# Performance work log

Measured on AMD Instinct MI355X. Metric: run time of the kernel, lower is better.

The kernel has to match this reference:

```python
import jax, jax.numpy as jnp
import numpy as np

# dims
T, B = 1024, 64
IN, EMB, HID, K, OUT = 32, 64, 128, 16, 32


def setup_inputs() -> dict:
    key = jax.random.key(0)
    ks = jax.random.split(key, 16)
    s = 0.05
    f32 = jnp.float32
    return {
        "inputs": jax.random.normal(ks[0], (T, B, IN), f32),
        "W_emb": jax.random.normal(ks[1], (IN, EMB), f32) * s,
        "b_emb": jnp.zeros((EMB,), f32),
        # layer 0: gates packed as [i, o, c, d]
        "Wx0": jax.random.normal(ks[2], (EMB, 4 * HID), f32) * s,
        "Wh0": jax.random.normal(ks[3], (HID, 4 * HID), f32) * s,
        "b0": jnp.zeros((4 * HID,), f32),
        "Wo0": jax.random.normal(ks[4], (HID, HID), f32) * s,
        "bo0": jnp.zeros((HID,), f32),
        # layer 1 (last layer projects to output_size)
        "Wx1": jax.random.normal(ks[5], (HID, 4 * HID), f32) * s,
        "Wh1": jax.random.normal(ks[6], (HID, 4 * HID), f32) * s,
        "b1": jnp.zeros((4 * HID,), f32),
        "Wo1": jax.random.normal(ks[7], (HID, OUT), f32) * s,
        "bo1": jnp.zeros((OUT,), f32),
    }


def mlstm_layer(x_seq, Wx, Wh, b, Wo, bo):
    """One mLSTM layer scanned over time.

    x_seq: [T, B, Din]. Cell state is a k-truncated fractional filter:
      c_t = sum_{j=0}^{K-1} w_j(d_t) * hc_{t-j},  hc = i ⊙ tanh(c_gate)
      w_0 = 1, w_j = w_{j-1} * (j-1+d_t)/j   (coeffs of (1-B)^{-d})
      d_t = 0.5 * sigmoid(d_gate)  in (0, 0.5)
    """
    H = Wh.shape[0]
    Bsz = x_seq.shape[1]
    xg = x_seq @ Wx + b  # [T, B, 4H] input contribution, precomputed once
    j = jnp.arange(1, K, dtype=x_seq.dtype).reshape(K - 1, 1, 1)

    h0 = jnp.zeros((Bsz, H), x_seq.dtype)
    buf0 = jnp.zeros((K, Bsz, H), x_seq.dtype)  # newest candidate first

    def step(carry, xg_t):
        h, buf = carry
        g = xg_t + h @ Wh
        i_g, o_g, c_g, d_g = jnp.split(g, 4, axis=-1)
        i_g = jax.nn.sigmoid(i_g)
        o_g = jax.nn.sigmoid(o_g)
        d = 0.5 * jax.nn.sigmoid(d_g)            # [B, H] dynamic memory param
        hc = i_g * jnp.tanh(c_g)                 # gated candidate
        buf = jnp.concatenate([hc[None], buf[:-1]], axis=0)  # [K, B, H]
        # fractional-integration weights w_j(d), recursive product, vectorized
        w = jnp.concatenate(
            [jnp.ones((1, Bsz, H), buf.dtype),
             jnp.cumprod((j - 1.0 + d) / j, axis=0)], axis=0)  # [K, B, H]
        c = jnp.sum(w * buf, axis=0)
        h_new = o_g * jnp.tanh(c)
        out = h_new @ Wo + bo
        return (h_new, buf), out

    _, outs = jax.lax.scan(step, (h0, buf0), xg)
    return outs  # [T, B, Dout]


def reference(inputs, W_emb, b_emb, Wx0, Wh0, b0, Wo0, bo0, Wx1, Wh1, b1, Wo1, bo1):
    x = inputs @ W_emb + b_emb                    # input embedding
    x = mlstm_layer(x, Wx0, Wh0, b0, Wo0, bo0)    # layer 0 -> hidden_size
    return mlstm_layer(x, Wx1, Wh1, b1, Wo1, bo1) # layer 1 -> output_size
```

## Files before the change

### kernel.cpp

```cpp
#include <hip/hip_runtime.h>
#include <hip/hip_bf16.h>
#include <cstdint>
#include <type_traits>

#define T_DIM 1024
#define B_DIM 64
#define IN_DIM 32
#define EMB_DIM 64
#define HID_DIM 128
#define K_TAPS 16
#define OUT_DIM 32
#define G4 (4*HID_DIM)
#define MROWS (T_DIM*B_DIM)

typedef _Float16 half8 __attribute__((ext_vector_type(8)));
typedef _Float16 half4 __attribute__((ext_vector_type(4)));
typedef float f32x4 __attribute__((ext_vector_type(4)));

#define MFMA16(a,b,c) __builtin_amdgcn_mfma_f32_16x16x32_f16((a),(b),(c),0,0,0)

__device__ __forceinline__ float fast_sigmoid(float x) {
    return __builtin_amdgcn_rcpf(1.0f + __expf(-x));
}
__device__ __forceinline__ float fast_tanh(float x) {
    return 1.0f - 2.0f * __builtin_amdgcn_rcpf(1.0f + __expf(2.0f * x));
}

__global__ void gemm_small(const float* __restrict__ A, const float* __restrict__ Bm,
                           float* __restrict__ C, int K2)
{
    int i = blockIdx.x, j = threadIdx.x;
    float acc = 0.f;
    for (int k = 0; k < K2; ++k) acc += A[i * K2 + k] * Bm[k * G4 + j];
    C[i * G4 + j] = acc;
}

__global__ void bias_comb(const float* __restrict__ bvec, const float* __restrict__ Bm,
                          const float* __restrict__ badd, float* __restrict__ bc, int K2)
{
    int j = threadIdx.x;
    float acc = badd[j];
    for (int k = 0; k < K2; ++k) acc += bvec[k] * Bm[k * G4 + j];
    bc[j] = acc;
}

template<int KK, int NCOLS, int NSTR, typename TA>
__global__ __launch_bounds__(256) void gemm_mfma(
    const TA* __restrict__ A, const float* __restrict__ W,
    const float* __restrict__ bias, float* __restrict__ C)
{
    constexpr int KT = KK / 32;
    constexpr int NT = NCOLS / 16;
    const int bm = blockIdx.x, bn = blockIdx.y;
    const int tid = threadIdx.x;
    const int w = tid >> 6, l = tid & 63, lc = l & 15, lk = l >> 4;

    __shared__ __align__(16) _Float16 aLds[64][KK + 8];

    if constexpr (std::is_same_v<TA, float>) {
        const float* Ab = A + (size_t)bm * 64 * KK;
        for (int idx = tid * 4; idx < 64 * KK; idx += 1024) {
            const int r = idx / KK, k = idx % KK;
            float4 v = *(const float4*)&Ab[idx];
            half4 h; h[0] = (_Float16)v.x; h[1] = (_Float16)v.y;
            h[2] = (_Float16)v.z; h[3] = (_Float16)v.w;
            *(half4*)&aLds[r][k] = h;
        }
    } else {
        const _Float16* Ab = (const _Float16*)A + (size_t)bm * 64 * KK;
        for (int idx = tid * 8; idx < 64 * KK; idx += 2048) {
            const int r = idx / KK, k = idx % KK;
            *(half8*)&aLds[r][k] = *(const half8*)&Ab[idx];
        }
    }

    half8 bf[NT][KT];
#pragma unroll
    for (int nt = 0; nt < NT; ++nt)
#pragma unroll
        for (int kt = 0; kt < KT; ++kt) {
            half8 v;
#pragma unroll
            for (int e = 0; e < 8; ++e)
                v[e] = (_Float16)W[(size_t)(kt * 32 + lk * 8 + e) * NSTR + bn * NCOLS + nt * 16 + lc];
            bf[nt][kt] = v;
        }

    __syncthreads();

    half8 af[KT];
#pragma unroll
    for (int kt = 0; kt < KT; ++kt)
        af[kt] = *(const half8*)&aLds[w * 16 + lc][kt * 32 + lk * 8];

    f32x4 acc[NT];
#pragma unroll
    for (int nt = 0; nt < NT; ++nt) acc[nt] = (f32x4){0.f, 0.f, 0.f, 0.f};
#pragma unroll
    for (int nt = 0; nt < NT; ++nt)
#pragma unroll
        for (int kt = 0; kt < KT; ++kt)
            acc[nt] = MFMA16(af[kt], bf[nt][kt], acc[nt]);

#pragma unroll
    for (int nt = 0; nt < NT; ++nt) {
        const int col = bn * NCOLS + nt * 16 + lc;
        const float bv = bias[col];
#pragma unroll
        for (int r = 0; r < 4; ++r) {
            const int row = bm * 64 + w * 16 + lk * 4 + r;
            C[(size_t)row * NSTR + col] = acc[nt][r] + bv;
        }
    }
}

__global__ __launch_bounds__(512) void scan_kernel(
    const float* __restrict__ XG, const float* __restrict__ Wh,
    _Float16* __restrict__ HoutH)
{
    const int b = blockIdx.x;
    const int tid = threadIdx.x;
    const int w = tid >> 6, l = tid & 63, lc = l & 15, lk = l >> 4;
    const int hid = w * 16 + lc;

    __shared__ __align__(16) _Float16 hbuf[2][HID_DIM];

    half8 bf[4][4];
#pragma unroll
    for (int gt = 0; gt < 4; ++gt)
#pragma unroll
        for (int kt = 0; kt < 4; ++kt) {
            half8 v;
#pragma unroll
            for (int e = 0; e < 8; ++e)
                v[e] = (_Float16)Wh[(size_t)(kt * 32 + lk * 8 + e) * G4 + gt * 128 + hid];
            bf[gt][kt] = v;
        }

    float rb[K_TAPS];
#pragma unroll
    for (int p = 0; p < K_TAPS; ++p) rb[p] = 0.f;

    if (tid < HID_DIM) { hbuf[0][tid] = (_Float16)0.f; hbuf[1][tid] = (_Float16)0.f; }
    __syncthreads();

    const float* xgb = XG + (size_t)b * G4;
    float xgp[2][4];
#pragma unroll
    for (int gt = 0; gt < 4; ++gt) xgp[0][gt] = xgb[gt * 128 + hid];
#pragma unroll
    for (int gt = 0; gt < 4; ++gt) xgp[1][gt] = xgb[(size_t)(B_DIM * G4) + gt * 128 + hid];

    for (int tb = 0; tb < T_DIM; tb += K_TAPS) {
#pragma unroll
        for (int p = 0; p < K_TAPS; ++p) {
            const int t = tb + p;
            half8 af0 = *(const half8*)&hbuf[p & 1][ 0 + lk * 8];
            half8 af1 = *(const half8*)&hbuf[p & 1][32 + lk * 8];
            half8 af2 = *(const half8*)&hbuf[p & 1][64 + lk * 8];
            half8 af3 = *(const half8*)&hbuf[p & 1][96 + lk * 8];
            f32x4 a0 = (f32x4){0.f,0.f,0.f,0.f}, a1 = a0, a2 = a0, a3 = a0;
            a0 = MFMA16(af0, bf[0][0], a0); a0 = MFMA16(af1, bf[0][1], a0);
            a0 = MFMA16(af2, bf[0][2], a0); a0 = MFMA16(af3, bf[0][3], a0);
            a1 = MFMA16(af0, bf[1][0], a1); a1 = MFMA16(af1, bf[1][1], a1);
            a1 = MFMA16(af2, bf[1][2], a1); a1 = MFMA16(af3, bf[1][3], a1);
            a2 = MFMA16(af0, bf[2][0], a2); a2 = MFMA16(af1, bf[2][1], a2);
            a2 = MFMA16(af2, bf[2][2], a2); a2 = MFMA16(af3, bf[2][3], a2);
            a3 = MFMA16(af0, bf[3][0], a3); a3 = MFMA16(af1, bf[3][1], a3);
            a3 = MFMA16(af2, bf[3][2], a3); a3 = MFMA16(af3, bf[3][3], a3);

            const float gi = xgp[p & 1][0] + a0[0];
            const float go = xgp[p & 1][1] + a1[0];
            const float gc = xgp[p & 1][2] + a2[0];
            const float gd = xgp[p & 1][3] + a3[0];

            if (t + 2 < T_DIM) {
#pragma unroll
                for (int gt = 0; gt < 4; ++gt)
                    xgp[p & 1][gt] = xgb[(size_t)(t + 2) * (B_DIM * G4) + gt * 128 + hid];
            }

            const float ig = fast_sigmoid(gi);
            const float og = fast_sigmoid(go);
            const float d  = 0.5f * fast_sigmoid(gd);
            const float hc = ig * fast_tanh(gc);
            rb[p] = hc;
            float c = hc, wj = 1.f;
#pragma unroll
            for (int jj = 1; jj < K_TAPS; ++jj) {
                wj *= (jj - 1.0f + d) * (1.0f / jj);
                c = fmaf(wj, rb[(p - jj) & (K_TAPS - 1)], c);
            }
            const float hn = og * fast_tanh(c);

            if (lk == 0) {
                hbuf[(p & 1) ^ 1][hid] = (_Float16)hn;
                HoutH[(size_t)t * (B_DIM * HID_DIM) + b * HID_DIM + hid] = (_Float16)hn;
            }
            __syncthreads();
        }
    }
}

extern "C" void kernel_launch(void* const* d_in, const int* in_sizes, int n_in,
                              void* d_out, int out_size, void* d_ws, size_t ws_size,
                              hipStream_t stream)
{
    const float* inputs = (const float*)d_in[0];
    const float* W_emb  = (const float*)d_in[1];
    const float* b_emb  = (const float*)d_in[2];
    const float* Wx0    = (const float*)d_in[3];
    const float* Wh0    = (const float*)d_in[4];
    const float* b0     = (const float*)d_in[5];
    const float* Wo0    = (const float*)d_in[6];
    const float* bo0    = (const float*)d_in[7];
    const float* Wx1    = (const float*)d_in[8];
    const float* Wh1    = (const float*)d_in[9];
    const float* b1     = (const float*)d_in[10];
    const float* Wo1    = (const float*)d_in[11];
    const float* bo1    = (const float*)d_in[12];
    float* out = (float*)d_out;

    float* ws = (float*)d_ws;
    float*     XG    = ws;
    _Float16*  HoutH = (_Float16*)(ws + (size_t)MROWS * G4);
    float*     W0c   = (float*)((char*)HoutH + (size_t)MROWS * HID_DIM * sizeof(_Float16));
    float*     b0c   = W0c + IN_DIM * G4;
    float*     W1c   = b0c + G4;
    float*     b1c   = W1c + HID_DIM * G4;

    gemm_small<<<IN_DIM, G4, 0, stream>>>(W_emb, Wx0, W0c, EMB_DIM);
    bias_comb<<<1, G4, 0, stream>>>(b_emb, Wx0, b0, b0c, EMB_DIM);
    gemm_mfma<IN_DIM, 64, G4, float>
        <<<dim3(MROWS / 64, G4 / 64), 256, 0, stream>>>(inputs, W0c, b0c, XG);
    scan_kernel<<<B_DIM, 512, 0, stream>>>(XG, Wh0, HoutH);

    gemm_small<<<HID_DIM, G4, 0, stream>>>(Wo0, Wx1, W1c, HID_DIM);
    bias_comb<<<1, G4, 0, stream>>>(bo0, Wx1, b1, b1c, HID_DIM);
    gemm_mfma<HID_DIM, 64, G4, _Float16>
        <<<dim3(MROWS / 64, G4 / 64), 256, 0, stream>>>(HoutH, W1c, b1c, XG);
    scan_kernel<<<B_DIM, 512, 0, stream>>>(XG, Wh1, HoutH);

    gemm_mfma<HID_DIM, OUT_DIM, OUT_DIM, _Float16>
        <<<dim3(MROWS / 64, 1), 256, 0, stream>>>(HoutH, Wo1, bo1, out);
}
```

Baseline: 1.506 ms.

## Shorten scan step critical path with independent MFMAs, tree sums and lighter barrier

```diff
diff --git a/kernel.cpp b/kernel.cpp
--- a/kernel.cpp
+++ b/kernel.cpp
@@ -26,6 +26,13 @@
     return 1.0f - 2.0f * __builtin_amdgcn_rcpf(1.0f + __expf(2.0f * x));
 }
 
+__device__ __forceinline__ void step_barrier() {
+    __builtin_amdgcn_sched_barrier(0);
+    asm volatile("s_waitcnt lgkmcnt(0)" ::: "memory");
+    __builtin_amdgcn_s_barrier();
+    __builtin_amdgcn_sched_barrier(0);
+}
+
 __global__ void gemm_small(const float* __restrict__ A, const float* __restrict__ Bm,
                            float* __restrict__ C, int K2)
 {
@@ -114,7 +121,7 @@
     }
 }
 
-__global__ __launch_bounds__(512) void scan_kernel(
+__global__ __launch_bounds__(512, 2) void scan_kernel(
     const float* __restrict__ XG, const float* __restrict__ Wh,
     _Float16* __restrict__ HoutH)
 {
@@ -145,11 +152,12 @@
     __syncthreads();
 
     const float* xgb = XG + (size_t)b * G4;
-    float xgp[2][4];
-#pragma unroll
-    for (int gt = 0; gt < 4; ++gt) xgp[0][gt] = xgb[gt * 128 + hid];
-#pragma unroll
-    for (int gt = 0; gt < 4; ++gt) xgp[1][gt] = xgb[(size_t)(B_DIM * G4) + gt * 128 + hid];
+    float xgp[4][4];
+#pragma unroll
+    for (int s = 0; s < 4; ++s)
+#pragma unroll
+        for (int gt = 0; gt < 4; ++gt)
+            xgp[s][gt] = xgb[(size_t)s * (B_DIM * G4) + gt * 128 + hid];
 
     for (int tb = 0; tb < T_DIM; tb += K_TAPS) {
 #pragma unroll
@@ -159,25 +167,25 @@
             half8 af1 = *(const half8*)&hbuf[p & 1][32 + lk * 8];
             half8 af2 = *(const half8*)&hbuf[p & 1][64 + lk * 8];
             half8 af3 = *(const half8*)&hbuf[p & 1][96 + lk * 8];
-            f32x4 a0 = (f32x4){0.f,0.f,0.f,0.f}, a1 = a0, a2 = a0, a3 = a0;
-            a0 = MFMA16(af0, bf[0][0], a0); a0 = MFMA16(af1, bf[0][1], a0);
-            a0 = MFMA16(af2, bf[0][2], a0); a0 = MFMA16(af3, bf[0][3], a0);
-            a1 = MFMA16(af0, bf[1][0], a1); a1 = MFMA16(af1, bf[1][1], a1);
-            a1 = MFMA16(af2, bf[1][2], a1); a1 = MFMA16(af3, bf[1][3], a1);
-            a2 = MFMA16(af0, bf[2][0], a2); a2 = MFMA16(af1, bf[2][1], a2);
-            a2 = MFMA16(af2, bf[2][2], a2); a2 = MFMA16(af3, bf[2][3], a2);
-            a3 = MFMA16(af0, bf[3][0], a3); a3 = MFMA16(af1, bf[3][1], a3);
-            a3 = MFMA16(af2, bf[3][2], a3); a3 = MFMA16(af3, bf[3][3], a3);
-
-            const float gi = xgp[p & 1][0] + a0[0];
-            const float go = xgp[p & 1][1] + a1[0];
-            const float gc = xgp[p & 1][2] + a2[0];
-            const float gd = xgp[p & 1][3] + a3[0];
-
-            if (t + 2 < T_DIM) {
+
+            const f32x4 z = (f32x4){0.f, 0.f, 0.f, 0.f};
+            f32x4 q[4][4];
+#pragma unroll
+            for (int gt = 0; gt < 4; ++gt) {
+                q[gt][0] = MFMA16(af0, bf[gt][0], z);
+                q[gt][1] = MFMA16(af1, bf[gt][1], z);
+                q[gt][2] = MFMA16(af2, bf[gt][2], z);
+                q[gt][3] = MFMA16(af3, bf[gt][3], z);
+            }
+            const float gi = xgp[p & 3][0] + ((q[0][0][0] + q[0][1][0]) + (q[0][2][0] + q[0][3][0]));
+            const float go = xgp[p & 3][1] + ((q[1][0][0] + q[1][1][0]) + (q[1][2][0] + q[1][3][0]));
+            const float gc = xgp[p & 3][2] + ((q[2][0][0] + q[2][1][0]) + (q[2][2][0] + q[2][3][0]));
+            const float gd = xgp[p & 3][3] + ((q[3][0][0] + q[3][1][0]) + (q[3][2][0] + q[3][3][0]));
+
+            if (t + 4 < T_DIM) {
 #pragma unroll
                 for (int gt = 0; gt < 4; ++gt)
-                    xgp[p & 1][gt] = xgb[(size_t)(t + 2) * (B_DIM * G4) + gt * 128 + hid];
+                    xgp[p & 3][gt] = xgb[(size_t)(t + 4) * (B_DIM * G4) + gt * 128 + hid];
             }
 
             const float ig = fast_sigmoid(gi);
@@ -185,19 +193,28 @@
             const float d  = 0.5f * fast_sigmoid(gd);
             const float hc = ig * fast_tanh(gc);
             rb[p] = hc;
-            float c = hc, wj = 1.f;
+
+            float term[K_TAPS];
+            term[0] = hc;
+            float wprod = 1.f;
 #pragma unroll
             for (int jj = 1; jj < K_TAPS; ++jj) {
-                wj *= (jj - 1.0f + d) * (1.0f / jj);
-                c = fmaf(wj, rb[(p - jj) & (K_TAPS - 1)], c);
-            }
+                wprod *= (jj - 1.0f + d) * (1.0f / jj);
+                term[jj] = wprod * rb[(p - jj) & (K_TAPS - 1)];
+            }
+            float s01 = (term[0] + term[1])   + (term[2] + term[3]);
+            float s23 = (term[4] + term[5])   + (term[6] + term[7]);
+            float s45 = (term[8] + term[9])   + (term[10] + term[11]);
+            float s67 = (term[12] + term[13]) + (term[14] + term[15]);
+            const float c = (s01 + s23) + (s45 + s67);
+
             const float hn = og * fast_tanh(c);
 
             if (lk == 0) {
                 hbuf[(p & 1) ^ 1][hid] = (_Float16)hn;
                 HoutH[(size_t)t * (B_DIM * HID_DIM) + b * HID_DIM + hid] = (_Float16)hn;
             }
-            __syncthreads();
+            step_barrier();
         }
     }
 }
```

New measurement: 1.614 ms. 7.2% more time.
